# Kernel tuning notes

Measured on AMD Instinct MI355X. Metric: run time of the kernel, lower is better.

Reference implementation:

```python
import jax, jax.numpy as jnp
import numpy as np

HEADS = 12
DIM_HEAD = 64
SCALE = DIM_HEAD ** -0.5


def setup_inputs() -> dict:
    key = jax.random.key(0)
    ks = jax.random.split(key, 5)
    b, n, dim = 16, 1024, 768
    inner = HEADS * DIM_HEAD  # 768
    x = jax.random.normal(ks[0], (b, n, dim), dtype=jnp.float32)
    w_qv = jax.random.normal(ks[1], (dim, 2 * inner), dtype=jnp.float32) * (dim ** -0.5)
    ext_k = jax.random.normal(ks[2], (1, HEADS, n, DIM_HEAD), dtype=jnp.float32)
    ext_bias = jax.random.normal(ks[3], (1, HEADS, n, n), dtype=jnp.float32)
    w_out = jax.random.normal(ks[4], (inner, dim), dtype=jnp.float32) * (inner ** -0.5)
    b_out = jnp.zeros((dim,), dtype=jnp.float32)
    return {"x": x, "w_qv": w_qv, "ext_k": ext_k, "ext_bias": ext_bias,
            "w_out": w_out, "b_out": b_out}


def reference(x, w_qv, ext_k, ext_bias, w_out, b_out):
    b, n, _ = x.shape
    qv = x @ w_qv                                   # [b, n, 2*inner]
    q, v = jnp.split(qv, 2, axis=-1)
    # b n (h d) -> b h n d
    q = q.reshape(b, n, HEADS, DIM_HEAD).transpose(0, 2, 1, 3)
    v = v.reshape(b, n, HEADS, DIM_HEAD).transpose(0, 2, 1, 3)
    # dots = (q @ ext_k^T + ext_bias) * scale       # [b, h, n, n]
    dots = (jnp.einsum('bhnd,ohmd->bhnm', q, ext_k) + ext_bias) * SCALE
    attn = jax.nn.softmax(dots, axis=-1)
    out = jnp.einsum('bhnm,bhmd->bhnd', attn, v)    # [b, h, n, d]
    out = out.transpose(0, 2, 1, 3).reshape(b, n, HEADS * DIM_HEAD)
    return out @ w_out + b_out
```

## Files before the change

### kernel.cpp

```cpp
#include <hip/hip_runtime.h>
#include <hip/hip_bf16.h>
#include <stdint.h>

typedef __bf16 bf16;
typedef short  s16x8 __attribute__((ext_vector_type(8)));
typedef float  f32x4 __attribute__((ext_vector_type(4)));

#define NHEADS  12
#define QKSCALE 0.125f

__device__ __forceinline__ void gload_lds16(const void* g, void* l) {
  __builtin_amdgcn_global_load_lds(
      (__attribute__((address_space(1))) void*)(g),
      (__attribute__((address_space(3))) void*)(l), 16, 0, 0);
}

__device__ __forceinline__ short bf16bits(float f) {
  union { bf16 h; short s; } u;
  u.h = (bf16)f;
  return u.s;
}
__device__ __forceinline__ float bfu2f(unsigned short u) {
  union { unsigned int i; float f; } c;
  c.i = ((unsigned int)u) << 16;
  return c.f;
}

__global__ __launch_bounds__(256) void cast4_kernel(const float* __restrict__ in,
                                                    bf16* __restrict__ out,
                                                    int n4, float scale) {
  int i = blockIdx.x * 256 + threadIdx.x;
  if (i >= n4) return;
  float4 v = ((const float4*)in)[i];
  union { bf16 h[4]; uint64_t u; } o;
  o.h[0] = (bf16)(v.x * scale);
  o.h[1] = (bf16)(v.y * scale);
  o.h[2] = (bf16)(v.z * scale);
  o.h[3] = (bf16)(v.w * scale);
  ((uint64_t*)out)[i] = o.u;
}

__global__ __launch_bounds__(256) void castT_tiled(const float* __restrict__ in,
                                                   bf16* __restrict__ out,
                                                   int R, int C) {
  __shared__ float tile[32][33];
  const int nbx = C >> 5;
  const int bx = blockIdx.x % nbx, by = blockIdx.x / nbx;
  const int tx = threadIdx.x & 31, ty = threadIdx.x >> 5;
  const int r0 = by << 5, c0 = bx << 5;
#pragma unroll
  for (int i = 0; i < 4; ++i)
    tile[ty + i * 8][tx] = in[(size_t)(r0 + ty + i * 8) * C + c0 + tx];
  __syncthreads();
#pragma unroll
  for (int i = 0; i < 4; ++i)
    out[(size_t)(c0 + ty + i * 8) * R + r0 + tx] = (bf16)tile[tx][ty + i * 8];
}

template <int EPI>
__global__ __launch_bounds__(256) void gemm128(const bf16* __restrict__ A,
                                               const bf16* __restrict__ BT,
                                               int M, int N, int K,
                                               bf16* __restrict__ outQ,
                                               bf16* __restrict__ outV,
                                               float* __restrict__ outC,
                                               const float* __restrict__ bias) {
  __shared__ char sA[8192];
  __shared__ char sB[8192];
  const int nb = N >> 7;
  const int bx = blockIdx.x % nb, by = blockIdx.x / nb;
  const int brow = by << 7, bcol = bx << 7;
  const int t = threadIdx.x;
  const int w = t >> 6, l = t & 63;
  const int wr = w >> 1, wc = w & 1;
  const int lr = l & 15, lg = l >> 4;

  const f32x4 fz = {0.f, 0.f, 0.f, 0.f};
  f32x4 acc[4][4];
#pragma unroll
  for (int m = 0; m < 4; ++m)
#pragma unroll
    for (int n = 0; n < 4; ++n) acc[m][n] = fz;

  const int nk = K >> 5;
  for (int kt = 0; kt < nk; ++kt) {
#pragma unroll
    for (int i = 0; i < 2; ++i) {
      int chunk = ((i * 4 + w) << 6) + l;
      int rrow = chunk >> 2, rc = chunk & 3;
      gload_lds16(A + (size_t)(brow + rrow) * K + (kt << 5) + (rc << 3),
                  sA + ((i * 4 + w) << 10));
      gload_lds16(BT + (size_t)(bcol + rrow) * K + (kt << 5) + (rc << 3),
                  sB + ((i * 4 + w) << 10));
    }
    __syncthreads();
    s16x8 af[4], bfr[4];
#pragma unroll
    for (int m = 0; m < 4; ++m)
      af[m] = *(const s16x8*)(sA + ((wr << 6) + (m << 4) + lr) * 64 + (lg << 4));
#pragma unroll
    for (int n = 0; n < 4; ++n)
      bfr[n] = *(const s16x8*)(sB + ((wc << 6) + (n << 4) + lr) * 64 + (lg << 4));
#pragma unroll
    for (int m = 0; m < 4; ++m)
#pragma unroll
      for (int n = 0; n < 4; ++n)
        acc[m][n] = __builtin_amdgcn_mfma_f32_16x16x32_bf16(af[m], bfr[n], acc[m][n], 0, 0, 0);
    __syncthreads();
  }

  if (EPI == 0) {
#pragma unroll
    for (int n = 0; n < 4; ++n) {
      int gcol = bcol + (wc << 6) + (n << 4) + lr;
      bf16* dst;
      int h, d;
      float sc;
      if (gcol < 768) { h = gcol >> 6; d = gcol & 63; dst = outQ; sc = QKSCALE; }
      else { int c2 = gcol - 768; h = c2 >> 6; d = c2 & 63; dst = outV; sc = 1.0f; }
#pragma unroll
      for (int m = 0; m < 4; ++m) {
        int growb = brow + (wr << 6) + (m << 4) + (lg << 2);
#pragma unroll
        for (int r = 0; r < 4; ++r) {
          int grow = growb + r;
          int b = grow >> 10, nr = grow & 1023;
          dst[(((size_t)(b * NHEADS + h) << 10) + nr) * 64 + d] = (bf16)(acc[m][n][r] * sc);
        }
      }
    }
  } else {
#pragma unroll
    for (int n = 0; n < 4; ++n) {
      int gcol = bcol + (wc << 6) + (n << 4) + lr;
      float bv = bias[gcol];
#pragma unroll
      for (int m = 0; m < 4; ++m) {
        int growb = brow + (wr << 6) + (m << 4) + (lg << 2);
#pragma unroll
        for (int r = 0; r < 4; ++r)
          outC[(size_t)(growb + r) * N + gcol] = acc[m][n][r] + bv;
      }
    }
  }
}

__global__ __launch_bounds__(256) void attn_kernel(const bf16* __restrict__ Q,
                                                   const bf16* __restrict__ V,
                                                   const bf16* __restrict__ Kx,
                                                   const bf16* __restrict__ Bias,
                                                   bf16* __restrict__ O) {
  __shared__ char sK[2][8192];
  __shared__ char sVT[2][8192];
  __shared__ char sP[4][2048];

  const int blk = blockIdx.x;
  const int b  = blk & 15;
  const int qb = (blk >> 4) & 15;
  const int h  = blk >> 8;
  const int bh = b * NHEADS + h;
  const int t = threadIdx.x, w = t >> 6, l = t & 63;
  const int lr = l & 15, lg = l >> 4;
  const int q0 = (qb << 6) + (w << 4);
  const size_t qvbase = (size_t)bh << 10;

  s16x8 qf[2];
#pragma unroll
  for (int kf = 0; kf < 2; ++kf)
    qf[kf] = *(const s16x8*)(Q + ((qvbase + q0 + lr) << 6) + (kf << 5) + (lg << 3));

  const f32x4 fz = {0.f, 0.f, 0.f, 0.f};
  f32x4 acc_o[4];
#pragma unroll
  for (int of = 0; of < 4; ++of) acc_o[of] = fz;
  float lsum = 0.f;

  const bf16* Kh = Kx + ((size_t)h << 16);
  const bf16* Brow = Bias + ((size_t)((h << 10) + q0 + lr)) * 1024;
  const bf16* Vb = V + (qvbase << 6);

  const int vr = l;
  const int vc0a = (w << 3), vc0b = (w << 3) + 32;
  uint4 va, vb2;

#define STAGE_K(kt_, buf_)                                                  \
  {                                                                         \
    _Pragma("unroll") for (int i = 0; i < 2; ++i) {                         \
      int rowloc = ((i * 4 + w) << 3) + (l >> 3);                           \
      int chunk = (l & 7) ^ (rowloc & 7);                                   \
      gload_lds16(Kh + ((((kt_) << 6) + rowloc) << 6) + (chunk << 3),       \
                  sK[buf_] + ((i * 4 + w) << 10));                          \
    }                                                                       \
  }
#define LOAD_V(kt_)                                                         \
  {                                                                         \
    const bf16* p_ = Vb + (((kt_) << 6) + vr) * 64;                         \
    va = *(const uint4*)(p_ + vc0a);                                        \
    vb2 = *(const uint4*)(p_ + vc0b);                                       \
  }
#define WRITE_VT(buf_)                                                      \
  {                                                                         \
    const bf16* pa_ = (const bf16*)&va;                                     \
    const bf16* pb_ = (const bf16*)&vb2;                                    \
    _Pragma("unroll") for (int e = 0; e < 8; ++e) {                         \
      int d_ = vc0a + e;                                                    \
      int off_ = (d_ << 7) + ((((vr >> 3) ^ (d_ & 7)) << 4) | ((vr & 7) << 1)); \
      *(bf16*)(sVT[buf_] + off_) = pa_[e];                                  \
    }                                                                       \
    _Pragma("unroll") for (int e = 0; e < 8; ++e) {                         \
      int d_ = vc0b + e;                                                    \
      int off_ = (d_ << 7) + ((((vr >> 3) ^ (d_ & 7)) << 4) | ((vr & 7) << 1)); \
      *(bf16*)(sVT[buf_] + off_) = pb_[e];                                  \
    }                                                                       \
  }

  STAGE_K(0, 0);
  LOAD_V(0);
  WRITE_VT(0);
  __syncthreads();

  for (int kt = 0; kt < 16; ++kt) {
    const int cur = kt & 1, nxt = cur ^ 1;
    if (kt < 15) {
      STAGE_K(kt + 1, nxt);
      LOAD_V(kt + 1);
    }

    float bfv[4][4];
#pragma unroll
    for (int cf = 0; cf < 4; ++cf) {
      ushort4 bu = *(const ushort4*)(Brow + (kt << 6) + (cf << 4) + (lg << 2));
      bfv[cf][0] = bfu2f(bu.x);
      bfv[cf][1] = bfu2f(bu.y);
      bfv[cf][2] = bfu2f(bu.z);
      bfv[cf][3] = bfu2f(bu.w);
    }

    f32x4 s[4];
    __builtin_amdgcn_s_setprio(1);
#pragma unroll
    for (int cf = 0; cf < 4; ++cf) {
      int kvloc = (cf << 4) + lr;
      f32x4 z = {bfv[cf][0], bfv[cf][1], bfv[cf][2], bfv[cf][3]};
#pragma unroll
      for (int kf = 0; kf < 2; ++kf) {
        int chunk = ((kf << 2) + lg) ^ (kvloc & 7);
        s16x8 kb8 = *(const s16x8*)(sK[cur] + (kvloc << 7) + (chunk << 4));
        z = __builtin_amdgcn_mfma_f32_16x16x32_bf16(kb8, qf[kf], z, 0, 0, 0);
      }
      s[cf] = z;
    }
    __builtin_amdgcn_s_setprio(0);

    float psum = 0.f;
#pragma unroll
    for (int cf = 0; cf < 4; ++cf)
#pragma unroll
      for (int r = 0; r < 4; ++r) {
        float p = __expf(s[cf][r]);
        s[cf][r] = p;
        psum += p;
      }
    lsum += psum;

#pragma unroll
    for (int cf = 0; cf < 4; ++cf) {
      ushort4 pk;
      pk.x = (unsigned short)bf16bits(s[cf][0]);
      pk.y = (unsigned short)bf16bits(s[cf][1]);
      pk.z = (unsigned short)bf16bits(s[cf][2]);
      pk.w = (unsigned short)bf16bits(s[cf][3]);
      int kvbyte = (cf << 5) + (lg << 3);
      int off = (lr << 7) + ((((kvbyte >> 4) ^ (lr & 7)) << 4) | (kvbyte & 15));
      *(ushort4*)(sP[w] + off) = pk;
    }
    s16x8 pa[2];
#pragma unroll
    for (int kf2 = 0; kf2 < 2; ++kf2) {
      int chunk = ((kf2 << 2) + lg) ^ (lr & 7);
      pa[kf2] = *(const s16x8*)(sP[w] + (lr << 7) + (chunk << 4));
    }

    __builtin_amdgcn_s_setprio(1);
#pragma unroll
    for (int of = 0; of < 4; ++of) {
      int d = (of << 4) + lr;
#pragma unroll
      for (int kf2 = 0; kf2 < 2; ++kf2) {
        int chunk = ((kf2 << 2) + lg) ^ (d & 7);
        s16x8 vbf = *(const s16x8*)(sVT[cur] + (d << 7) + (chunk << 4));
        acc_o[of] = __builtin_amdgcn_mfma_f32_16x16x32_bf16(pa[kf2], vbf, acc_o[of], 0, 0, 0);
      }
    }
    __builtin_amdgcn_s_setprio(0);

    if (kt < 15) WRITE_VT(nxt);
    __syncthreads();
  }

  lsum += __shfl_xor(lsum, 16);
  lsum += __shfl_xor(lsum, 32);
  float inv[4];
#pragma unroll
  for (int r = 0; r < 4; ++r)
    inv[r] = 1.0f / __shfl(lsum, (lg << 4) + (lg << 2) + r);
#pragma unroll
  for (int of = 0; of < 4; ++of)
#pragma unroll
    for (int r = 0; r < 4; ++r) {
      int qrow = q0 + (lg << 2) + r;
      size_t off = ((size_t)((b << 10) + qrow)) * 768 + (h << 6) + (of << 4) + lr;
      O[off] = (bf16)(acc_o[of][r] * inv[r]);
    }
#undef STAGE_K
#undef LOAD_V
#undef WRITE_VT
}

extern "C" void kernel_launch(void* const* d_in, const int* in_sizes, int n_in,
                              void* d_out, int out_size, void* d_ws, size_t ws_size,
                              hipStream_t stream) {
  const float* x        = (const float*)d_in[0];
  const float* w_qv     = (const float*)d_in[1];
  const float* ext_k    = (const float*)d_in[2];
  const float* ext_bias = (const float*)d_in[3];
  const float* w_out    = (const float*)d_in[4];
  const float* b_out    = (const float*)d_in[5];
  float* out = (float*)d_out;

  char* ws = (char*)d_ws;
  bf16* xb    = (bf16*)(ws);
  bf16* wqvT  = (bf16*)(ws + 25165824);
  bf16* kb    = (bf16*)(ws + 27525120);
  bf16* wobT  = (bf16*)(ws + 29097984);
  bf16* biasb = (bf16*)(ws + 30277632);
  bf16* qws   = (bf16*)(ws + 55443456);
  bf16* vws   = (bf16*)(ws + 80609280);
  bf16* attout = xb;

  cast4_kernel<<<12288, 256, 0, stream>>>(x, xb, 3145728, 1.0f);
  cast4_kernel<<<12288, 256, 0, stream>>>(ext_bias, biasb, 3145728, QKSCALE);
  cast4_kernel<<<768, 256, 0, stream>>>(ext_k, kb, 196608, 1.0f);
  castT_tiled<<<1152, 256, 0, stream>>>(w_qv, wqvT, 768, 1536);
  castT_tiled<<<576, 256, 0, stream>>>(w_out, wobT, 768, 768);

  gemm128<0><<<1536, 256, 0, stream>>>(xb, wqvT, 16384, 1536, 768, qws, vws, nullptr, nullptr);
  attn_kernel<<<3072, 256, 0, stream>>>(qws, vws, kb, biasb, attout);
  gemm128<1><<<768, 256, 0, stream>>>(attout, wobT, 16384, 768, 768, nullptr, nullptr, out, b_out);
}
```

Measured before the change: 408.7 us.

## Emit V transposed from QV GEMM and stage it via direct LDS loads

The QV projection epilogue now writes V in a per-head transposed layout [b,h,d,n] using packed 4-element stores. The attention kernel then fills the V^T tile in shared memory with async global-to-LDS loads, the same way it fills K, instead of doing register loads followed by scattered 2-byte LDS writes. The bias loads are also prefetched one tile ahead into registers. This removes per-iteration LDS transpose work and exposes the load latency to overlap, at the cost of strided 8-byte stores in the GEMM epilogue.

```diff
diff --git a/kernel.cpp b/kernel.cpp
--- a/kernel.cpp
+++ b/kernel.cpp
@@ -62,7 +62,7 @@
                                                const bf16* __restrict__ BT,
                                                int M, int N, int K,
                                                bf16* __restrict__ outQ,
-                                               bf16* __restrict__ outV,
+                                               bf16* __restrict__ outVT,
                                                float* __restrict__ outC,
                                                const float* __restrict__ bias) {
   __shared__ char sA[8192];
@@ -113,19 +113,32 @@
 #pragma unroll
     for (int n = 0; n < 4; ++n) {
       int gcol = bcol + (wc << 6) + (n << 4) + lr;
-      bf16* dst;
-      int h, d;
-      float sc;
-      if (gcol < 768) { h = gcol >> 6; d = gcol & 63; dst = outQ; sc = QKSCALE; }
-      else { int c2 = gcol - 768; h = c2 >> 6; d = c2 & 63; dst = outV; sc = 1.0f; }
-#pragma unroll
-      for (int m = 0; m < 4; ++m) {
-        int growb = brow + (wr << 6) + (m << 4) + (lg << 2);
-#pragma unroll
-        for (int r = 0; r < 4; ++r) {
-          int grow = growb + r;
-          int b = grow >> 10, nr = grow & 1023;
-          dst[(((size_t)(b * NHEADS + h) << 10) + nr) * 64 + d] = (bf16)(acc[m][n][r] * sc);
+      if (gcol < 768) {
+        int h = gcol >> 6, d = gcol & 63;
+#pragma unroll
+        for (int m = 0; m < 4; ++m) {
+          int growb = brow + (wr << 6) + (m << 4) + (lg << 2);
+#pragma unroll
+          for (int r = 0; r < 4; ++r) {
+            int grow = growb + r;
+            int b = grow >> 10, nr = grow & 1023;
+            outQ[(((size_t)(b * NHEADS + h) << 10) + nr) * 64 + d] =
+                (bf16)(acc[m][n][r] * QKSCALE);
+          }
+        }
+      } else {
+        int c2 = gcol - 768;
+        int h = c2 >> 6, d = c2 & 63;
+#pragma unroll
+        for (int m = 0; m < 4; ++m) {
+          int growb = brow + (wr << 6) + (m << 4) + (lg << 2);
+          int b = growb >> 10, nr0 = growb & 1023;
+          ushort4 pk;
+          pk.x = (unsigned short)bf16bits(acc[m][n][0]);
+          pk.y = (unsigned short)bf16bits(acc[m][n][1]);
+          pk.z = (unsigned short)bf16bits(acc[m][n][2]);
+          pk.w = (unsigned short)bf16bits(acc[m][n][3]);
+          *(ushort4*)(outVT + ((((size_t)(b * NHEADS + h) << 6) + d) << 10) + nr0) = pk;
         }
       }
     }
@@ -146,7 +159,7 @@
 }
 
 __global__ __launch_bounds__(256) void attn_kernel(const bf16* __restrict__ Q,
-                                                   const bf16* __restrict__ V,
+                                                   const bf16* __restrict__ VT,
                                                    const bf16* __restrict__ Kx,
                                                    const bf16* __restrict__ Bias,
                                                    bf16* __restrict__ O) {
@@ -177,11 +190,7 @@
 
   const bf16* Kh = Kx + ((size_t)h << 16);
   const bf16* Brow = Bias + ((size_t)((h << 10) + q0 + lr)) * 1024;
-  const bf16* Vb = V + (qvbase << 6);
-
-  const int vr = l;
-  const int vc0a = (w << 3), vc0b = (w << 3) + 32;
-  uint4 va, vb2;
+  const bf16* Vth = VT + (qvbase << 6);
 
 #define STAGE_K(kt_, buf_)                                                  \
   {                                                                         \
@@ -192,48 +201,38 @@
                   sK[buf_] + ((i * 4 + w) << 10));                          \
     }                                                                       \
   }
-#define LOAD_V(kt_)                                                         \
+#define STAGE_VT(kt_, buf_)                                                 \
   {                                                                         \
-    const bf16* p_ = Vb + (((kt_) << 6) + vr) * 64;                         \
-    va = *(const uint4*)(p_ + vc0a);                                        \
-    vb2 = *(const uint4*)(p_ + vc0b);                                       \
-  }
-#define WRITE_VT(buf_)                                                      \
-  {                                                                         \
-    const bf16* pa_ = (const bf16*)&va;                                     \
-    const bf16* pb_ = (const bf16*)&vb2;                                    \
-    _Pragma("unroll") for (int e = 0; e < 8; ++e) {                         \
-      int d_ = vc0a + e;                                                    \
-      int off_ = (d_ << 7) + ((((vr >> 3) ^ (d_ & 7)) << 4) | ((vr & 7) << 1)); \
-      *(bf16*)(sVT[buf_] + off_) = pa_[e];                                  \
+    _Pragma("unroll") for (int i = 0; i < 2; ++i) {                         \
+      int rowloc = ((i * 4 + w) << 3) + (l >> 3);          \
+      int chunk = (l & 7) ^ (rowloc & 7);                                   \
+      gload_lds16(Vth + ((size_t)rowloc << 10) + ((kt_) << 6) + (chunk << 3), \
+                  sVT[buf_] + ((i * 4 + w) << 10));                         \
     }                                                                       \
-    _Pragma("unroll") for (int e = 0; e < 8; ++e) {                         \
-      int d_ = vc0b + e;                                                    \
-      int off_ = (d_ << 7) + ((((vr >> 3) ^ (d_ & 7)) << 4) | ((vr & 7) << 1)); \
-      *(bf16*)(sVT[buf_] + off_) = pb_[e];                                  \
-    }                                                                       \
   }
 
   STAGE_K(0, 0);
-  LOAD_V(0);
-  WRITE_VT(0);
+  STAGE_VT(0, 0);
+  ushort4 bu_cur[4];
+#pragma unroll
+  for (int cf = 0; cf < 4; ++cf)
+    bu_cur[cf] = *(const ushort4*)(Brow + (cf << 4) + (lg << 2));
   __syncthreads();
 
   for (int kt = 0; kt < 16; ++kt) {
     const int cur = kt & 1, nxt = cur ^ 1;
     if (kt < 15) {
       STAGE_K(kt + 1, nxt);
-      LOAD_V(kt + 1);
+      STAGE_VT(kt + 1, nxt);
     }
 
     float bfv[4][4];
 #pragma unroll
     for (int cf = 0; cf < 4; ++cf) {
-      ushort4 bu = *(const ushort4*)(Brow + (kt << 6) + (cf << 4) + (lg << 2));
-      bfv[cf][0] = bfu2f(bu.x);
-      bfv[cf][1] = bfu2f(bu.y);
-      bfv[cf][2] = bfu2f(bu.z);
-      bfv[cf][3] = bfu2f(bu.w);
+      bfv[cf][0] = bfu2f(bu_cur[cf].x);
+      bfv[cf][1] = bfu2f(bu_cur[cf].y);
+      bfv[cf][2] = bfu2f(bu_cur[cf].z);
+      bfv[cf][3] = bfu2f(bu_cur[cf].w);
     }
 
     f32x4 s[4];
@@ -281,6 +280,12 @@
       pa[kf2] = *(const s16x8*)(sP[w] + (lr << 7) + (chunk << 4));
     }
 
+    if (kt < 15) {
+#pragma unroll
+      for (int cf = 0; cf < 4; ++cf)
+        bu_cur[cf] = *(const ushort4*)(Brow + ((kt + 1) << 6) + (cf << 4) + (lg << 2));
+    }
+
     __builtin_amdgcn_s_setprio(1);
 #pragma unroll
     for (int of = 0; of < 4; ++of) {
@@ -294,7 +299,6 @@
     }
     __builtin_amdgcn_s_setprio(0);
 
-    if (kt < 15) WRITE_VT(nxt);
     __syncthreads();
   }
 
@@ -313,8 +317,7 @@
       O[off] = (bf16)(acc_o[of][r] * inv[r]);
     }
 #undef STAGE_K
-#undef LOAD_V
-#undef WRITE_VT
+#undef STAGE_VT
 }
 
 extern "C" void kernel_launch(void* const* d_in, const int* in_sizes, int n_in,
@@ -335,7 +338,7 @@
   bf16* wobT  = (bf16*)(ws + 29097984);
   bf16* biasb = (bf16*)(ws + 30277632);
   bf16* qws   = (bf16*)(ws + 55443456);
-  bf16* vws   = (bf16*)(ws + 80609280);
+  bf16* vtws  = (bf16*)(ws + 80609280);
   bf16* attout = xb;
 
   cast4_kernel<<<12288, 256, 0, stream>>>(x, xb, 3145728, 1.0f);
@@ -344,7 +347,7 @@
   castT_tiled<<<1152, 256, 0, stream>>>(w_qv, wqvT, 768, 1536);
   castT_tiled<<<576, 256, 0, stream>>>(w_out, wobT, 768, 768);
 
-  gemm128<0><<<1536, 256, 0, stream>>>(xb, wqvT, 16384, 1536, 768, qws, vws, nullptr, nullptr);
-  attn_kernel<<<3072, 256, 0, stream>>>(qws, vws, kb, biasb, attout);
+  gemm128<0><<<1536, 256, 0, stream>>>(xb, wqvT, 16384, 1536, 768, qws, vtws, nullptr, nullptr);
+  attn_kernel<<<3072, 256, 0, stream>>>(qws, vtws, kb, biasb, attout);
   gemm128<1><<<768, 256, 0, stream>>>(attout, wobT, 16384, 768, 768, nullptr, nullptr, out, b_out);
 }
```

New measurement: 387.4 us. 1.05x faster.
